# Performance work log

Hardware: AMD Instinct MI355X
Metric: run time of the kernel (lower is better)

Reference implementation:

```python
import jax, jax.numpy as jnp
import numpy as np

EPS = 1e-5  # torch LayerNorm default
H = 8       # num_heads


def _ln(x, w, b):
    mu = jnp.mean(x, axis=-1, keepdims=True)
    var = jnp.mean(jnp.square(x - mu), axis=-1, keepdims=True)
    return (x - mu) * jax.lax.rsqrt(var + EPS) * w + b


def setup_inputs() -> dict:
    key = jax.random.key(0)
    ks = jax.random.split(key, 8)
    B, N, C = 4, 2048, 512
    d_ff = 4 * C
    g = lambda k, shape: jax.random.normal(k, shape, jnp.float32) * 0.02
    return {
        "x": jax.random.normal(ks[0], (B, N, C), jnp.float32),
        "e": jax.random.normal(ks[1], (B, N, C), jnp.float32),
        "w_qkv": g(ks[2], (C, 3 * C)),
        "w_s": g(ks[3], (C, C)),
        "w_gate": g(ks[4], (C, C)),
        "w_proj": g(ks[5], (C, C)),
        "b_proj": jnp.zeros((C,), jnp.float32),
        "ln1_w": jnp.ones((C,), jnp.float32), "ln1_b": jnp.zeros((C,), jnp.float32),
        "ln2_w": jnp.ones((C,), jnp.float32), "ln2_b": jnp.zeros((C,), jnp.float32),
        "ln3_w": jnp.ones((C,), jnp.float32), "ln3_b": jnp.zeros((C,), jnp.float32),
        "w_fc1": g(ks[6], (C, d_ff)), "b_fc1": jnp.zeros((d_ff,), jnp.float32),
        "w_fc2": g(ks[7], (d_ff, C)), "b_fc2": jnp.zeros((C,), jnp.float32),
    }


def reference(x, e, w_qkv, w_s, w_gate, w_proj, b_proj,
              ln1_w, ln1_b, ln2_w, ln2_b, ln3_w, ln3_b,
              w_fc1, b_fc1, w_fc2, b_fc2):
    B, N, C = x.shape
    D = C // H
    scale = D ** -0.5  # qk_scale=None -> (dim//num_heads)**-0.5

    # --- attention branch: x + attn(norm1(x), norm2(e)) ---
    xn = _ln(x, ln1_w, ln1_b)
    en = _ln(e, ln2_w, ln2_b)
    qkv = (xn @ w_qkv).reshape(B, N, 3, H, D).transpose(2, 0, 3, 1, 4)  # [3,B,H,N,D]
    q, k, v = qkv[0], qkv[1], qkv[2]
    s = (en @ w_s).reshape(B, N, H, D).transpose(0, 2, 1, 3)            # [B,H,N,D]
    attn = jax.nn.softmax(jnp.einsum('bhnd,bhmd->bhnm', q, k + s) * scale, axis=-1)
    o = jnp.einsum('bhnm,bhmd->bhnd', attn, v).transpose(0, 2, 1, 3).reshape(B, N, C)
    o = (o * (xn @ w_gate)) @ w_proj + b_proj
    x = x + o  # drop_path is identity (drop_prob=0)

    # --- MLP branch: x + mlp(norm3(x)) ---
    xn3 = _ln(x, ln3_w, ln3_b)
    h = jax.nn.gelu(xn3 @ w_fc1 + b_fc1, approximate=False)  # torch nn.GELU = exact erf
    return x + (h @ w_fc2 + b_fc2)
```

## Files before the change

kernel.cpp:

```cpp
#include <hip/hip_runtime.h>

typedef unsigned short u16;
typedef short s16;
typedef u16 u16x4 __attribute__((ext_vector_type(4)));
typedef u16 u16x8 __attribute__((ext_vector_type(8)));
typedef s16 s16x8 __attribute__((ext_vector_type(8)));
typedef float f32x4 __attribute__((ext_vector_type(4)));

__device__ __forceinline__ float b2f(u16 u) {
  union { unsigned int i; float f; } v;
  v.i = ((unsigned int)u) << 16;
  return v.f;
}
__device__ __forceinline__ u16 f2b(float f) {
  union { float f; unsigned int i; } v;
  v.f = f;
  unsigned int r = v.i + 0x7fffu + ((v.i >> 16) & 1u);
  return (u16)(r >> 16);
}

#define MFMA16(a, b, c) __builtin_amdgcn_mfma_f32_16x16x32_bf16(a, b, c, 0, 0, 0)

__device__ __forceinline__ void gld16(const u16* g, u16* l) {
  __builtin_amdgcn_global_load_lds(
      (const __attribute__((address_space(1))) void*)g,
      (__attribute__((address_space(3))) void*)l, 16, 0, 0);
}

__global__ __launch_bounds__(256) void ln_kernel(const float* __restrict__ inv,
                                                 const float* __restrict__ w,
                                                 const float* __restrict__ bvec,
                                                 u16* __restrict__ out) {
  const int row = blockIdx.x * 4 + (threadIdx.x >> 6);
  const int lane = threadIdx.x & 63;
  const float* p = inv + (size_t)row * 512 + lane * 8;
  f32x4 v0 = *(const f32x4*)p;
  f32x4 v1 = *(const f32x4*)(p + 4);
  float x[8];
#pragma unroll
  for (int i = 0; i < 4; i++) { x[i] = v0[i]; x[4 + i] = v1[i]; }
  float s = 0.f;
#pragma unroll
  for (int i = 0; i < 8; i++) s += x[i];
#pragma unroll
  for (int m = 1; m < 64; m <<= 1) s += __shfl_xor(s, m, 64);
  const float mu = s * (1.0f / 512.0f);
  float vs = 0.f;
#pragma unroll
  for (int i = 0; i < 8; i++) { const float d = x[i] - mu; vs += d * d; }
#pragma unroll
  for (int m = 1; m < 64; m <<= 1) vs += __shfl_xor(vs, m, 64);
  const float r = rsqrtf(vs * (1.0f / 512.0f) + 1e-5f);
  const f32x4 w0 = *(const f32x4*)(w + lane * 8);
  const f32x4 w1 = *(const f32x4*)(w + lane * 8 + 4);
  const f32x4 b0 = *(const f32x4*)(bvec + lane * 8);
  const f32x4 b1 = *(const f32x4*)(bvec + lane * 8 + 4);
  u16x8 ov;
#pragma unroll
  for (int i = 0; i < 4; i++) {
    ov[i] = f2b((x[i] - mu) * r * w0[i] + b0[i]);
    ov[4 + i] = f2b((x[4 + i] - mu) * r * w1[i] + b1[i]);
  }
  *(u16x8*)(out + (size_t)row * 512 + lane * 8) = ov;
}

__global__ __launch_bounds__(256) void transp_kernel(const float* __restrict__ src,
                                                     u16* __restrict__ dst,
                                                     int K, int N) {
  __shared__ float T[64][65];
  const int n0 = blockIdx.x * 64, k0 = blockIdx.y * 64;
  const int c = threadIdx.x & 63, r0 = threadIdx.x >> 6;
#pragma unroll
  for (int i = 0; i < 16; i++) {
    const int r = i * 4 + r0;
    T[r][c] = src[(size_t)(k0 + r) * N + n0 + c];
  }
  __syncthreads();
#pragma unroll
  for (int i = 0; i < 16; i++) {
    const int r = i * 4 + r0;
    dst[(size_t)(n0 + r) * K + k0 + c] = f2b(T[c][r]);
  }
}

enum { EPI_NONE = 0, EPI_F32RES = 1, EPI_GELU = 2 };

template<int EPI, int BM>
__global__ __launch_bounds__(256) void mgemm(const u16* __restrict__ A,
                                             const u16* __restrict__ Bt,
                                             int M, int N, int K,
                                             u16* __restrict__ Cb, float* Cf,
                                             const float* __restrict__ bias,
                                             const float* resf) {
  constexpr int NT = (BM == 128) ? 4 : 2;
  constexpr int ACH = BM / 32;
  __shared__ u16 As[BM * 64];
  __shared__ u16 Bs[128 * 64];
  const int tid = threadIdx.x;
  const int wv = tid >> 6, lane = tid & 63;
  const int quad = lane >> 4, l16 = lane & 15;
  const int wrow = (BM == 128) ? (wv >> 1) * 64 : 0;
  const int wcol = (BM == 128) ? (wv & 1) * 64 : wv * 32;
  const int m0 = blockIdx.y * BM, n0 = blockIdx.x * 128;
  const int lrow = lane >> 3, lcol = (lane & 7) * 8;
  f32x4 acc[4][NT];
#pragma unroll
  for (int i = 0; i < 4; i++)
#pragma unroll
    for (int j = 0; j < NT; j++) acc[i][j] = (f32x4){0.f, 0.f, 0.f, 0.f};
  for (int k0 = 0; k0 < K; k0 += 64) {
    __syncthreads();
#pragma unroll
    for (int i = 0; i < ACH; i++) {
      const int ch = wv * ACH + i;
      gld16(A + (size_t)(m0 + ch * 8 + lrow) * K + k0 + lcol, &As[ch * 512]);
    }
#pragma unroll
    for (int i = 0; i < 4; i++) {
      const int ch = wv * 4 + i;
      gld16(Bt + (size_t)(n0 + ch * 8 + lrow) * K + k0 + lcol, &Bs[ch * 512]);
    }
    __syncthreads();
#pragma unroll
    for (int ks = 0; ks < 2; ks++) {
      s16x8 af[4], bf[NT];
#pragma unroll
      for (int mt = 0; mt < 4; mt++)
        af[mt] = *(const s16x8*)&As[(wrow + mt * 16 + l16) * 64 + ks * 32 + quad * 8];
#pragma unroll
      for (int nt = 0; nt < NT; nt++)
        bf[nt] = *(const s16x8*)&Bs[(wcol + nt * 16 + l16) * 64 + ks * 32 + quad * 8];
#pragma unroll
      for (int mt = 0; mt < 4; mt++)
#pragma unroll
        for (int nt = 0; nt < NT; nt++)
          acc[mt][nt] = MFMA16(af[mt], bf[nt], acc[mt][nt]);
    }
  }
#pragma unroll
  for (int nt = 0; nt < NT; nt++) {
    const int n = n0 + wcol + nt * 16 + l16;
    const float bn = (EPI != EPI_NONE) ? bias[n] : 0.f;
#pragma unroll
    for (int mt = 0; mt < 4; mt++) {
#pragma unroll
      for (int r = 0; r < 4; r++) {
        const int m = m0 + wrow + mt * 16 + quad * 4 + r;
        float v = acc[mt][nt][r] + bn;
        if (EPI == EPI_GELU)
          v = 0.5f * v * (1.0f + erff(v * 0.70710678118654752f));
        if (EPI == EPI_F32RES) {
          const size_t idx = (size_t)m * N + n;
          Cf[idx] = v + resf[idx];
        } else {
          Cb[(size_t)m * N + n] = f2b(v);
        }
      }
    }
  }
}

__global__ __launch_bounds__(256) void ksvt_kernel(const u16* __restrict__ qkv,
                                                   const u16* __restrict__ sb,
                                                   u16* __restrict__ ksg,
                                                   u16* __restrict__ vtg) {
  __shared__ u16 T[64 * 72];
  const int bh = blockIdx.y;
  const int b = bh >> 3, h = bh & 7;
  const int kk0 = blockIdx.x * 64;
  const size_t rb = (size_t)b * 2048;
  const size_t base = (size_t)bh * 131072;
  const int row = threadIdx.x >> 2, cb = (threadIdx.x & 3) * 16;
  const u16* kp = qkv + (rb + kk0 + row) * 1536 + 512 + h * 64 + cb;
  const u16* sp = sb + (rb + kk0 + row) * 512 + h * 64 + cb;
  const u16x8 k0v = *(const u16x8*)kp;
  const u16x8 k1v = *(const u16x8*)(kp + 8);
  const u16x8 s0v = *(const u16x8*)sp;
  const u16x8 s1v = *(const u16x8*)(sp + 8);
  u16x8 o0, o1;
#pragma unroll
  for (int i = 0; i < 8; i++) {
    o0[i] = f2b(b2f(k0v[i]) + b2f(s0v[i]));
    o1[i] = f2b(b2f(k1v[i]) + b2f(s1v[i]));
  }
  *(u16x8*)(ksg + base + (size_t)(kk0 + row) * 64 + cb) = o0;
  *(u16x8*)(ksg + base + (size_t)(kk0 + row) * 64 + cb + 8) = o1;
  const u16x8 v0v = *(const u16x8*)(kp + 512);
  const u16x8 v1v = *(const u16x8*)(kp + 520);
  *(u16x8*)&T[row * 72 + cb] = v0v;
  *(u16x8*)&T[row * 72 + cb + 8] = v1v;
  __syncthreads();
  u16x8 a0, a1;
#pragma unroll
  for (int i = 0; i < 8; i++) {
    a0[i] = T[(cb + i) * 72 + row];
    a1[i] = T[(cb + 8 + i) * 72 + row];
  }
  *(u16x8*)(vtg + base + (size_t)row * 2048 + kk0 + cb) = a0;
  *(u16x8*)(vtg + base + (size_t)row * 2048 + kk0 + cb + 8) = a1;
}

__global__ __launch_bounds__(256) void attn_kernel(const u16* __restrict__ qkv,
                                                   const u16* __restrict__ ksg,
                                                   const u16* __restrict__ vtg,
                                                   u16* __restrict__ ob) {
  __shared__ u16 KSs[64 * 64];
  __shared__ u16 VTs[64 * 64];
  __shared__ u16 PS[4][16 * 72];
  const int tid = threadIdx.x;
  const int w = tid >> 6, lane = tid & 63;
  const int quad = lane >> 4, l16 = lane & 15;
  const int q0 = blockIdx.x * 64;
  const int bh = blockIdx.y;
  const int h = bh & 7;
  const size_t rb = (size_t)(bh >> 3) * 2048;
  const size_t base = (size_t)bh * 131072;
  const int lrow = lane >> 3, lcol = (lane & 7) * 8;

  s16x8 aq[2];
  {
    const u16* qp = qkv + (rb + q0 + w * 16 + l16) * 1536 + h * 64 + quad * 8;
#pragma unroll
    for (int ks = 0; ks < 2; ks++) {
      const u16x8 qv = *(const u16x8*)(qp + ks * 32);
      s16x8 t;
#pragma unroll
      for (int i = 0; i < 8; i++) t[i] = (s16)f2b(b2f(qv[i]) * 0.125f);
      aq[ks] = t;
    }
  }
  float m_run = -1e30f, l_run = 0.f;
  f32x4 oacc[4];
#pragma unroll
  for (int nt = 0; nt < 4; nt++) oacc[nt] = (f32x4){0.f, 0.f, 0.f, 0.f};

  for (int kt = 0; kt < 32; kt++) {
    const int kk0 = kt * 64;
    __syncthreads();
#pragma unroll
    for (int i = 0; i < 2; i++) {
      const int ch = w * 2 + i;
      gld16(ksg + base + (size_t)kk0 * 64 + ch * 512 + lane * 8, &KSs[ch * 512]);
      gld16(vtg + base + (size_t)(ch * 8 + lrow) * 2048 + kk0 + lcol, &VTs[ch * 512]);
    }
    __syncthreads();
    f32x4 sacc[4];
#pragma unroll
    for (int mt = 0; mt < 4; mt++) sacc[mt] = (f32x4){0.f, 0.f, 0.f, 0.f};
#pragma unroll
    for (int ks = 0; ks < 2; ks++) {
#pragma unroll
      for (int mt = 0; mt < 4; mt++) {
        const s16x8 kf = *(const s16x8*)&KSs[(mt * 16 + l16) * 64 + ks * 32 + quad * 8];
        sacc[mt] = MFMA16(kf, aq[ks], sacc[mt]);
      }
    }
    float lm = -1e30f;
#pragma unroll
    for (int mt = 0; mt < 4; mt++)
#pragma unroll
      for (int r = 0; r < 4; r++) lm = fmaxf(lm, sacc[mt][r]);
    lm = fmaxf(lm, __shfl_xor(lm, 16, 64));
    lm = fmaxf(lm, __shfl_xor(lm, 32, 64));
    const float mn = fmaxf(m_run, lm);
    const float alpha = __expf(m_run - mn);
    m_run = mn;
    float ls = 0.f;
#pragma unroll
    for (int mt = 0; mt < 4; mt++) {
#pragma unroll
      for (int r = 0; r < 4; r++) {
        const float pv = __expf(sacc[mt][r] - mn);
        sacc[mt][r] = pv;
        ls += pv;
      }
    }
    ls += __shfl_xor(ls, 16, 64);
    ls += __shfl_xor(ls, 32, 64);
    l_run = l_run * alpha + ls;
#pragma unroll
    for (int mt = 0; mt < 4; mt++) {
      u16x4 pk;
#pragma unroll
      for (int r = 0; r < 4; r++) pk[r] = f2b(sacc[mt][r]);
      *(u16x4*)&PS[w][l16 * 72 + mt * 16 + quad * 4] = pk;
    }
#pragma unroll
    for (int r = 0; r < 4; r++) {
      const float af = __shfl(alpha, quad * 4 + r, 64);
#pragma unroll
      for (int nt = 0; nt < 4; nt++) oacc[nt][r] *= af;
    }
#pragma unroll
    for (int ks = 0; ks < 2; ks++) {
      const s16x8 pf = *(const s16x8*)&PS[w][l16 * 72 + ks * 32 + quad * 8];
#pragma unroll
      for (int nt = 0; nt < 4; nt++) {
        const s16x8 vf = *(const s16x8*)&VTs[(nt * 16 + l16) * 64 + ks * 32 + quad * 8];
        oacc[nt] = MFMA16(pf, vf, oacc[nt]);
      }
    }
  }
  const float lq = __shfl(l_run, quad * 4 + (lane & 3), 64);
  (void)lq;
#pragma unroll
  for (int r = 0; r < 4; r++) {
    const float linv = 1.0f / __shfl(l_run, quad * 4 + r, 64);
    const size_t rowb = (rb + q0 + w * 16 + quad * 4 + r) * 512 + h * 64;
#pragma unroll
    for (int nt = 0; nt < 4; nt++)
      ob[rowb + nt * 16 + l16] = f2b(oacc[nt][r] * linv);
  }
}

__global__ __launch_bounds__(256) void ew_mul_kernel(const u16* __restrict__ a,
                                                     const u16* __restrict__ b,
                                                     u16* __restrict__ o) {
  const size_t idx = ((size_t)blockIdx.x * 256 + threadIdx.x) * 8;
  const u16x8 av = *(const u16x8*)(a + idx);
  const u16x8 bv = *(const u16x8*)(b + idx);
  u16x8 ov;
#pragma unroll
  for (int i = 0; i < 8; i++) ov[i] = f2b(b2f(av[i]) * b2f(bv[i]));
  *(u16x8*)(o + idx) = ov;
}

extern "C" void kernel_launch(void* const* d_in, const int* in_sizes, int n_in,
                              void* d_out, int out_size, void* d_ws, size_t ws_size,
                              hipStream_t stream) {
  const float* x      = (const float*)d_in[0];
  const float* e      = (const float*)d_in[1];
  const float* w_qkv  = (const float*)d_in[2];
  const float* w_s    = (const float*)d_in[3];
  const float* w_gate = (const float*)d_in[4];
  const float* w_proj = (const float*)d_in[5];
  const float* b_proj = (const float*)d_in[6];
  const float* ln1w   = (const float*)d_in[7];
  const float* ln1b   = (const float*)d_in[8];
  const float* ln2w   = (const float*)d_in[9];
  const float* ln2b   = (const float*)d_in[10];
  const float* ln3w   = (const float*)d_in[11];
  const float* ln3b   = (const float*)d_in[12];
  const float* w_fc1  = (const float*)d_in[13];
  const float* b_fc1  = (const float*)d_in[14];
  const float* w_fc2  = (const float*)d_in[15];
  const float* b_fc2  = (const float*)d_in[16];
  float* out = (float*)d_out;
  char* ws = (char*)d_ws;

  u16* xn    = (u16*)(ws + 0);
  u16* en    = (u16*)(ws + 8388608);
  u16* qkv   = (u16*)(ws + 16777216);
  u16* sbuf  = (u16*)(ws + 41943040);
  u16* gate  = (u16*)(ws + 50331648);
  u16* obuf  = (u16*)(ws + 58720256);
  u16* wqT   = (u16*)(ws + 67108864);
  u16* wsT   = (u16*)(ws + 68681728);
  u16* wgT   = (u16*)(ws + 69206016);
  u16* wpT   = (u16*)(ws + 69730304);
  u16* wf1T  = (u16*)(ws + 70254592);
  u16* wf2T  = (u16*)(ws + 72351744);
  u16* vtg   = (u16*)(ws + 74448896);
  u16* ksg   = en;
  u16* og    = en;
  u16* hbuf  = qkv;
  u16* xn3   = xn;

  dim3 blk(256);
  transp_kernel<<<dim3(24, 8), blk, 0, stream>>>(w_qkv, wqT, 512, 1536);
  transp_kernel<<<dim3(8, 8), blk, 0, stream>>>(w_s, wsT, 512, 512);
  transp_kernel<<<dim3(8, 8), blk, 0, stream>>>(w_gate, wgT, 512, 512);
  transp_kernel<<<dim3(8, 8), blk, 0, stream>>>(w_proj, wpT, 512, 512);
  transp_kernel<<<dim3(32, 8), blk, 0, stream>>>(w_fc1, wf1T, 512, 2048);
  transp_kernel<<<dim3(8, 32), blk, 0, stream>>>(w_fc2, wf2T, 2048, 512);

  ln_kernel<<<2048, blk, 0, stream>>>(x, ln1w, ln1b, xn);
  ln_kernel<<<2048, blk, 0, stream>>>(e, ln2w, ln2b, en);
  mgemm<EPI_NONE, 128><<<dim3(12, 64), blk, 0, stream>>>(
      xn, wqT, 8192, 1536, 512, qkv, nullptr, nullptr, nullptr);
  mgemm<EPI_NONE, 64><<<dim3(4, 128), blk, 0, stream>>>(
      en, wsT, 8192, 512, 512, sbuf, nullptr, nullptr, nullptr);
  ksvt_kernel<<<dim3(32, 32), blk, 0, stream>>>(qkv, sbuf, ksg, vtg);
  mgemm<EPI_NONE, 64><<<dim3(4, 128), blk, 0, stream>>>(
      xn, wgT, 8192, 512, 512, gate, nullptr, nullptr, nullptr);
  attn_kernel<<<dim3(32, 32), blk, 0, stream>>>(qkv, ksg, vtg, obuf);
  ew_mul_kernel<<<2048, blk, 0, stream>>>(obuf, gate, og);
  mgemm<EPI_F32RES, 64><<<dim3(4, 128), blk, 0, stream>>>(
      og, wpT, 8192, 512, 512, nullptr, out, b_proj, x);
  ln_kernel<<<2048, blk, 0, stream>>>(out, ln3w, ln3b, xn3);
  mgemm<EPI_GELU, 128><<<dim3(16, 64), blk, 0, stream>>>(
      xn3, wf1T, 8192, 2048, 512, hbuf, nullptr, b_fc1, nullptr);
  mgemm<EPI_F32RES, 64><<<dim3(4, 128), blk, 0, stream>>>(
      hbuf, wf2T, 8192, 512, 2048, nullptr, out, b_fc2, out);
  (void)in_sizes; (void)n_in; (void)out_size; (void)ws_size;
}
```

Baseline: 405.2 us.

## Fuse gate GEMM into QKV, gate multiply into attention, swizzle LDS, batch prep kernels

The gate projection weight is concatenated with the QKV weight so one wider GEMM produces q, k, v and gate. The elementwise gate multiply is folded into the attention epilogue, which removes a kernel and a round trip through memory. The six weight-transpose launches are merged into one kernel, and the two layernorms on x and e into another, to cut launch overhead. LDS tiles in the GEMM and attention kernels now use an XOR swizzle to reduce bank conflicts on fragment reads, at the cost of extra index arithmetic.

```diff
diff --git a/kernel.cpp b/kernel.cpp
--- a/kernel.cpp
+++ b/kernel.cpp
@@ -25,6 +25,49 @@
   __builtin_amdgcn_global_load_lds(
       (const __attribute__((address_space(1))) void*)g,
       (__attribute__((address_space(3))) void*)l, 16, 0, 0);
+}
+
+__global__ __launch_bounds__(256) void ln12_kernel(
+    const float* __restrict__ x, const float* __restrict__ e,
+    const float* __restrict__ w1, const float* __restrict__ b1,
+    const float* __restrict__ w2, const float* __restrict__ b2,
+    u16* __restrict__ xn, u16* __restrict__ en) {
+  int bid = blockIdx.x;
+  const float *inv, *w, *bb;
+  u16* out;
+  if (bid < 2048) { inv = x; w = w1; bb = b1; out = xn; }
+  else { bid -= 2048; inv = e; w = w2; bb = b2; out = en; }
+  const int row = bid * 4 + (threadIdx.x >> 6);
+  const int lane = threadIdx.x & 63;
+  const float* p = inv + (size_t)row * 512 + lane * 8;
+  f32x4 v0 = *(const f32x4*)p;
+  f32x4 v1 = *(const f32x4*)(p + 4);
+  float xv[8];
+#pragma unroll
+  for (int i = 0; i < 4; i++) { xv[i] = v0[i]; xv[4 + i] = v1[i]; }
+  float s = 0.f;
+#pragma unroll
+  for (int i = 0; i < 8; i++) s += xv[i];
+#pragma unroll
+  for (int m = 1; m < 64; m <<= 1) s += __shfl_xor(s, m, 64);
+  const float mu = s * (1.0f / 512.0f);
+  float vs = 0.f;
+#pragma unroll
+  for (int i = 0; i < 8; i++) { const float d = xv[i] - mu; vs += d * d; }
+#pragma unroll
+  for (int m = 1; m < 64; m <<= 1) vs += __shfl_xor(vs, m, 64);
+  const float r = rsqrtf(vs * (1.0f / 512.0f) + 1e-5f);
+  const f32x4 w0 = *(const f32x4*)(w + lane * 8);
+  const f32x4 w1v = *(const f32x4*)(w + lane * 8 + 4);
+  const f32x4 bb0 = *(const f32x4*)(bb + lane * 8);
+  const f32x4 bb1 = *(const f32x4*)(bb + lane * 8 + 4);
+  u16x8 ov;
+#pragma unroll
+  for (int i = 0; i < 4; i++) {
+    ov[i] = f2b((xv[i] - mu) * r * w0[i] + bb0[i]);
+    ov[4 + i] = f2b((xv[4 + i] - mu) * r * w1v[i] + bb1[i]);
+  }
+  *(u16x8*)(out + (size_t)row * 512 + lane * 8) = ov;
 }
 
 __global__ __launch_bounds__(256) void ln_kernel(const float* __restrict__ inv,
@@ -64,11 +107,22 @@
   *(u16x8*)(out + (size_t)row * 512 + lane * 8) = ov;
 }
 
-__global__ __launch_bounds__(256) void transp_kernel(const float* __restrict__ src,
-                                                     u16* __restrict__ dst,
-                                                     int K, int N) {
+__global__ __launch_bounds__(256) void wprep_kernel(
+    const float* __restrict__ wq, const float* __restrict__ wsc,
+    const float* __restrict__ wg, const float* __restrict__ wp,
+    const float* __restrict__ w1, const float* __restrict__ w2,
+    u16* __restrict__ wqgT, u16* __restrict__ wsT, u16* __restrict__ wpT,
+    u16* __restrict__ wf1T, u16* __restrict__ wf2T) {
   __shared__ float T[64][65];
-  const int n0 = blockIdx.x * 64, k0 = blockIdx.y * 64;
+  int bid = blockIdx.x;
+  const float* src; u16* dst; int K, N, ntiles;
+  if (bid < 192)      { src = wq;  dst = wqgT;              K = 512;  N = 1536; ntiles = 24; }
+  else if (bid < 256) { src = wg;  dst = wqgT + 1536 * 512; K = 512;  N = 512;  ntiles = 8; bid -= 192; }
+  else if (bid < 320) { src = wsc; dst = wsT;               K = 512;  N = 512;  ntiles = 8; bid -= 256; }
+  else if (bid < 384) { src = wp;  dst = wpT;               K = 512;  N = 512;  ntiles = 8; bid -= 320; }
+  else if (bid < 640) { src = w1;  dst = wf1T;              K = 512;  N = 2048; ntiles = 32; bid -= 384; }
+  else                { src = w2;  dst = wf2T;              K = 2048; N = 512;  ntiles = 8; bid -= 640; }
+  const int n0 = (bid % ntiles) * 64, k0 = (bid / ntiles) * 64;
   const int c = threadIdx.x & 63, r0 = threadIdx.x >> 6;
 #pragma unroll
   for (int i = 0; i < 16; i++) {
@@ -99,10 +153,12 @@
   const int tid = threadIdx.x;
   const int wv = tid >> 6, lane = tid & 63;
   const int quad = lane >> 4, l16 = lane & 15;
+  const int sw = l16 & 7;
   const int wrow = (BM == 128) ? (wv >> 1) * 64 : 0;
   const int wcol = (BM == 128) ? (wv & 1) * 64 : wv * 32;
   const int m0 = blockIdx.y * BM, n0 = blockIdx.x * 128;
-  const int lrow = lane >> 3, lcol = (lane & 7) * 8;
+  const int lrow = lane >> 3;
+  const int lcs = ((lane & 7) ^ lrow) * 8;
   f32x4 acc[4][NT];
 #pragma unroll
   for (int i = 0; i < 4; i++)
@@ -113,12 +169,12 @@
 #pragma unroll
     for (int i = 0; i < ACH; i++) {
       const int ch = wv * ACH + i;
-      gld16(A + (size_t)(m0 + ch * 8 + lrow) * K + k0 + lcol, &As[ch * 512]);
+      gld16(A + (size_t)(m0 + ch * 8 + lrow) * K + k0 + lcs, &As[ch * 512]);
     }
 #pragma unroll
     for (int i = 0; i < 4; i++) {
       const int ch = wv * 4 + i;
-      gld16(Bt + (size_t)(n0 + ch * 8 + lrow) * K + k0 + lcol, &Bs[ch * 512]);
+      gld16(Bt + (size_t)(n0 + ch * 8 + lrow) * K + k0 + lcs, &Bs[ch * 512]);
     }
     __syncthreads();
 #pragma unroll
@@ -126,10 +182,12 @@
       s16x8 af[4], bf[NT];
 #pragma unroll
       for (int mt = 0; mt < 4; mt++)
-        af[mt] = *(const s16x8*)&As[(wrow + mt * 16 + l16) * 64 + ks * 32 + quad * 8];
+        af[mt] = *(const s16x8*)&As[(wrow + mt * 16 + l16) * 64 +
+                                    (((ks * 4 + quad) ^ sw) * 8)];
 #pragma unroll
       for (int nt = 0; nt < NT; nt++)
-        bf[nt] = *(const s16x8*)&Bs[(wcol + nt * 16 + l16) * 64 + ks * 32 + quad * 8];
+        bf[nt] = *(const s16x8*)&Bs[(wcol + nt * 16 + l16) * 64 +
+                                    (((ks * 4 + quad) ^ sw) * 8)];
 #pragma unroll
       for (int mt = 0; mt < 4; mt++)
 #pragma unroll
@@ -160,7 +218,7 @@
   }
 }
 
-__global__ __launch_bounds__(256) void ksvt_kernel(const u16* __restrict__ qkv,
+__global__ __launch_bounds__(256) void ksvt_kernel(const u16* __restrict__ qg,
                                                    const u16* __restrict__ sb,
                                                    u16* __restrict__ ksg,
                                                    u16* __restrict__ vtg) {
@@ -171,7 +229,7 @@
   const size_t rb = (size_t)b * 2048;
   const size_t base = (size_t)bh * 131072;
   const int row = threadIdx.x >> 2, cb = (threadIdx.x & 3) * 16;
-  const u16* kp = qkv + (rb + kk0 + row) * 1536 + 512 + h * 64 + cb;
+  const u16* kp = qg + (rb + kk0 + row) * 2048 + 512 + h * 64 + cb;
   const u16* sp = sb + (rb + kk0 + row) * 512 + h * 64 + cb;
   const u16x8 k0v = *(const u16x8*)kp;
   const u16x8 k1v = *(const u16x8*)(kp + 8);
@@ -200,26 +258,28 @@
   *(u16x8*)(vtg + base + (size_t)row * 2048 + kk0 + cb + 8) = a1;
 }
 
-__global__ __launch_bounds__(256) void attn_kernel(const u16* __restrict__ qkv,
+__global__ __launch_bounds__(256) void attn_kernel(const u16* __restrict__ qg,
                                                    const u16* __restrict__ ksg,
                                                    const u16* __restrict__ vtg,
-                                                   u16* __restrict__ ob) {
+                                                   u16* __restrict__ og) {
   __shared__ u16 KSs[64 * 64];
   __shared__ u16 VTs[64 * 64];
   __shared__ u16 PS[4][16 * 72];
   const int tid = threadIdx.x;
   const int w = tid >> 6, lane = tid & 63;
   const int quad = lane >> 4, l16 = lane & 15;
+  const int sw = l16 & 7;
   const int q0 = blockIdx.x * 64;
   const int bh = blockIdx.y;
   const int h = bh & 7;
   const size_t rb = (size_t)(bh >> 3) * 2048;
   const size_t base = (size_t)bh * 131072;
-  const int lrow = lane >> 3, lcol = (lane & 7) * 8;
+  const int lrow = lane >> 3;
+  const int lcs = ((lane & 7) ^ lrow) * 8;
 
   s16x8 aq[2];
   {
-    const u16* qp = qkv + (rb + q0 + w * 16 + l16) * 1536 + h * 64 + quad * 8;
+    const u16* qp = qg + (rb + q0 + w * 16 + l16) * 2048 + h * 64 + quad * 8;
 #pragma unroll
     for (int ks = 0; ks < 2; ks++) {
       const u16x8 qv = *(const u16x8*)(qp + ks * 32);
@@ -240,8 +300,8 @@
 #pragma unroll
     for (int i = 0; i < 2; i++) {
       const int ch = w * 2 + i;
-      gld16(ksg + base + (size_t)kk0 * 64 + ch * 512 + lane * 8, &KSs[ch * 512]);
-      gld16(vtg + base + (size_t)(ch * 8 + lrow) * 2048 + kk0 + lcol, &VTs[ch * 512]);
+      gld16(ksg + base + (size_t)(kk0 + ch * 8 + lrow) * 64 + lcs, &KSs[ch * 512]);
+      gld16(vtg + base + (size_t)(ch * 8 + lrow) * 2048 + kk0 + lcs, &VTs[ch * 512]);
     }
     __syncthreads();
     f32x4 sacc[4];
@@ -251,7 +311,8 @@
     for (int ks = 0; ks < 2; ks++) {
 #pragma unroll
       for (int mt = 0; mt < 4; mt++) {
-        const s16x8 kf = *(const s16x8*)&KSs[(mt * 16 + l16) * 64 + ks * 32 + quad * 8];
+        const s16x8 kf = *(const s16x8*)&KSs[(mt * 16 + l16) * 64 +
+                                             (((ks * 4 + quad) ^ sw) * 8)];
         sacc[mt] = MFMA16(kf, aq[ks], sacc[mt]);
       }
     }
@@ -296,33 +357,23 @@
       const s16x8 pf = *(const s16x8*)&PS[w][l16 * 72 + ks * 32 + quad * 8];
 #pragma unroll
       for (int nt = 0; nt < 4; nt++) {
-        const s16x8 vf = *(const s16x8*)&VTs[(nt * 16 + l16) * 64 + ks * 32 + quad * 8];
+        const s16x8 vf = *(const s16x8*)&VTs[(nt * 16 + l16) * 64 +
+                                             (((ks * 4 + quad) ^ sw) * 8)];
         oacc[nt] = MFMA16(pf, vf, oacc[nt]);
       }
     }
   }
-  const float lq = __shfl(l_run, quad * 4 + (lane & 3), 64);
-  (void)lq;
 #pragma unroll
   for (int r = 0; r < 4; r++) {
     const float linv = 1.0f / __shfl(l_run, quad * 4 + r, 64);
+    const size_t grow = (rb + q0 + w * 16 + quad * 4 + r) * 2048 + 1536 + h * 64;
     const size_t rowb = (rb + q0 + w * 16 + quad * 4 + r) * 512 + h * 64;
 #pragma unroll
-    for (int nt = 0; nt < 4; nt++)
-      ob[rowb + nt * 16 + l16] = f2b(oacc[nt][r] * linv);
-  }
-}
-
-__global__ __launch_bounds__(256) void ew_mul_kernel(const u16* __restrict__ a,
-                                                     const u16* __restrict__ b,
-                                                     u16* __restrict__ o) {
-  const size_t idx = ((size_t)blockIdx.x * 256 + threadIdx.x) * 8;
-  const u16x8 av = *(const u16x8*)(a + idx);
-  const u16x8 bv = *(const u16x8*)(b + idx);
-  u16x8 ov;
-#pragma unroll
-  for (int i = 0; i < 8; i++) ov[i] = f2b(b2f(av[i]) * b2f(bv[i]));
-  *(u16x8*)(o + idx) = ov;
+    for (int nt = 0; nt < 4; nt++) {
+      const float g = b2f(qg[grow + nt * 16 + l16]);
+      og[rowb + nt * 16 + l16] = f2b(oacc[nt][r] * linv * g);
+    }
+  }
 }
 
 extern "C" void kernel_launch(void* const* d_in, const int* in_sizes, int n_in,
@@ -350,43 +401,31 @@
 
   u16* xn    = (u16*)(ws + 0);
   u16* en    = (u16*)(ws + 8388608);
-  u16* qkv   = (u16*)(ws + 16777216);
-  u16* sbuf  = (u16*)(ws + 41943040);
-  u16* gate  = (u16*)(ws + 50331648);
+  u16* qg    = (u16*)(ws + 16777216);
+  u16* sbuf  = (u16*)(ws + 50331648);
   u16* obuf  = (u16*)(ws + 58720256);
-  u16* wqT   = (u16*)(ws + 67108864);
-  u16* wsT   = (u16*)(ws + 68681728);
-  u16* wgT   = (u16*)(ws + 69206016);
+  u16* wqgT  = (u16*)(ws + 67108864);
+  u16* wsT   = (u16*)(ws + 69206016);
   u16* wpT   = (u16*)(ws + 69730304);
   u16* wf1T  = (u16*)(ws + 70254592);
   u16* wf2T  = (u16*)(ws + 72351744);
   u16* vtg   = (u16*)(ws + 74448896);
   u16* ksg   = en;
-  u16* og    = en;
-  u16* hbuf  = qkv;
+  u16* hbuf  = qg;
   u16* xn3   = xn;
 
   dim3 blk(256);
-  transp_kernel<<<dim3(24, 8), blk, 0, stream>>>(w_qkv, wqT, 512, 1536);
-  transp_kernel<<<dim3(8, 8), blk, 0, stream>>>(w_s, wsT, 512, 512);
-  transp_kernel<<<dim3(8, 8), blk, 0, stream>>>(w_gate, wgT, 512, 512);
-  transp_kernel<<<dim3(8, 8), blk, 0, stream>>>(w_proj, wpT, 512, 512);
-  transp_kernel<<<dim3(32, 8), blk, 0, stream>>>(w_fc1, wf1T, 512, 2048);
-  transp_kernel<<<dim3(8, 32), blk, 0, stream>>>(w_fc2, wf2T, 2048, 512);
-
-  ln_kernel<<<2048, blk, 0, stream>>>(x, ln1w, ln1b, xn);
-  ln_kernel<<<2048, blk, 0, stream>>>(e, ln2w, ln2b, en);
-  mgemm<EPI_NONE, 128><<<dim3(12, 64), blk, 0, stream>>>(
-      xn, wqT, 8192, 1536, 512, qkv, nullptr, nullptr, nullptr);
+  wprep_kernel<<<896, blk, 0, stream>>>(w_qkv, w_s, w_gate, w_proj, w_fc1, w_fc2,
+                                        wqgT, wsT, wpT, wf1T, wf2T);
+  ln12_kernel<<<4096, blk, 0, stream>>>(x, e, ln1w, ln1b, ln2w, ln2b, xn, en);
+  mgemm<EPI_NONE, 128><<<dim3(16, 64), blk, 0, stream>>>(
+      xn, wqgT, 8192, 2048, 512, qg, nullptr, nullptr, nullptr);
   mgemm<EPI_NONE, 64><<<dim3(4, 128), blk, 0, stream>>>(
       en, wsT, 8192, 512, 512, sbuf, nullptr, nullptr, nullptr);
-  ksvt_kernel<<<dim3(32, 32), blk, 0, stream>>>(qkv, sbuf, ksg, vtg);
-  mgemm<EPI_NONE, 64><<<dim3(4, 128), blk, 0, stream>>>(
-      xn, wgT, 8192, 512, 512, gate, nullptr, nullptr, nullptr);
-  attn_kernel<<<dim3(32, 32), blk, 0, stream>>>(qkv, ksg, vtg, obuf);
-  ew_mul_kernel<<<2048, blk, 0, stream>>>(obuf, gate, og);
+  ksvt_kernel<<<dim3(32, 32), blk, 0, stream>>>(qg, sbuf, ksg, vtg);
+  attn_kernel<<<dim3(32, 32), blk, 0, stream>>>(qg, ksg, vtg, obuf);
   mgemm<EPI_F32RES, 64><<<dim3(4, 128), blk, 0, stream>>>(
-      og, wpT, 8192, 512, 512, nullptr, out, b_proj, x);
+      obuf, wpT, 8192, 512, 512, nullptr, out, b_proj, x);
   ln_kernel<<<2048, blk, 0, stream>>>(out, ln3w, ln3b, xn3);
   mgemm<EPI_GELU, 128><<<dim3(16, 64), blk, 0, stream>>>(
       xn3, wf1T, 8192, 2048, 512, hbuf, nullptr, b_fc1, nullptr);
```

Result: faster. 351.1 us (-13.4%).
